# Performance work log

Hardware: AMD Instinct MI355X
Metric: run time of the kernel (lower is better)

## Reference

```python
import jax, jax.numpy as jnp
import numpy as np
from jax.scipy.special import logsumexp

D = 256; H = 8; A = D // H
B_CONST = 0.9; P_MAX = 50000.0; P_MIN = 1e-4; TANH_RATE = 0.005; EPS = 1e-10
SCALE = 1.0 / np.sqrt(D)


def setup_inputs() -> dict:
    key = jax.random.key(0)
    ks = jax.random.split(key, 5)
    B, S = 2, 512
    context = jax.random.normal(ks[0], (B, S, D), dtype=jnp.float32)
    W_Q = jax.random.normal(ks[1], (D, D), dtype=jnp.float32) * (1.0 / np.sqrt(D))
    W_KV = jax.random.normal(ks[2], (2 * D, D), dtype=jnp.float32) * (1.0 / np.sqrt(D))
    W_out = jax.random.normal(ks[3], (D, D), dtype=jnp.float32) * (1.0 / np.sqrt(D))
    p_param = jax.random.normal(ks[4], (D,), dtype=jnp.float32) * 0.02
    return {"context": context, "W_Q": W_Q, "W_KV": W_KV, "W_out": W_out, "p_param": p_param}


def reference(context, W_Q, W_KV, W_out, p_param):
    B, S, _ = context.shape
    # projections (nn.Linear: x @ W.T)
    q = context @ W_Q.T                          # [B,S,D]
    kv = context @ W_KV.T                        # [B,S,2D]
    k, v = kv[..., :D], kv[..., D:]
    # scaled p: p_max*tanh(tanh_rate*p)+1, then replace exact zeros with p_min
    p = P_MAX * jnp.tanh(TANH_RATE * p_param) + 1.0
    p = p + (p == 0).astype(p.dtype) * P_MIN
    # minmax-normalize v over the key/sequence axis into [b, 1]
    v_max = jnp.max(v, axis=-2, keepdims=True)   # [B,1,D]
    v_min = jnp.min(v, axis=-2, keepdims=True)
    v = (1.0 - B_CONST) * (v - v_min) / (v_max - v_min + EPS) + B_CONST
    z = p * jnp.log(v)                           # [B,S,D]
    # split heads
    qh = q.reshape(B, S, H, A).transpose(0, 2, 1, 3)          # [B,H,S,A]
    kh = k.reshape(B, S, H, A).transpose(0, 2, 1, 3)          # [B,H,S,A]
    zh = z.reshape(B, S, H, A).transpose(0, 2, 1, 3)[:, :, None]  # [B,H,1,K,A]
    dot = jnp.einsum('bhqa,bhka->bhqk', qh, kh)
    w = jax.nn.log_softmax(dot * SCALE, axis=-1)              # [B,H,Q,K]
    # log-domain power mean: logsumexp over keys of log-weights + p*log(v)
    mean = logsumexp(w[..., None] + zh, axis=-2)              # [B,H,Q,A]
    mean = mean.transpose(0, 2, 1, 3).reshape(B, S, D)
    e = jnp.exp(mean / p)
    # invert v minmax normalization
    e = (e - B_CONST) * (v_max - v_min + EPS) / (1.0 - B_CONST) + v_min
    return e @ W_out.T
```

## Files before the change

### kernel.cpp

```cpp
#include <hip/hip_runtime.h>
#include <math.h>

#define DD 256
#define HH 8
#define AA 32
#define SS 512
#define BB 2
constexpr float BCONST      = 0.9f;
constexpr float ONE_MINUS_B = 0.1f;
constexpr float EPSF        = 1e-10f;
constexpr float SCALEF      = 0.0625f;
constexpr float FLTMAX      = 3.402823466e38f;

#define OFF_QKV    0
#define OFF_VP     786432
#define OFF_EW     1048576
#define OFF_PMIN   1310720
#define OFF_PMAX   1318912
#define OFF_VMIN   1327104
#define OFF_VRANGE 1327616
#define OFF_P      1328128

template<int TM, int TN, int RM, int RN, bool MM>
__global__ __launch_bounds__(256) void gemm_t(
    const float* __restrict__ A, const float* __restrict__ B0,
    const float* __restrict__ B1, int nsplit,
    float* __restrict__ C, int ldc, int K, int lda,
    float* __restrict__ pminP, float* __restrict__ pmaxP) {
  constexpr int LDT = 36;
  constexpr int CG  = TN / RN;
  constexpr int NA  = TM * 32 / 1024;
  constexpr int NB  = TN * 32 / 1024;
  __shared__ float As[TM][LDT];
  __shared__ float Bs[TN][LDT];
  const int i0 = blockIdx.x * TM;
  const int j0 = blockIdx.y * TN;
  const float* Bsrc = (j0 < nsplit) ? (B0 + (size_t)j0 * K)
                                    : (B1 + (size_t)(j0 - nsplit) * K);
  const int t  = threadIdx.x;
  const int lr = t >> 3;
  const int lc = (t & 7) << 2;
  const int tx = t % CG, ty = t / CG;

  float4 pa[NA], pb[NB];
#pragma unroll
  for (int u = 0; u < NA; ++u)
    pa[u] = *(const float4*)(A + (size_t)(i0 + lr + 32 * u) * lda + lc);
#pragma unroll
  for (int u = 0; u < NB; ++u)
    pb[u] = *(const float4*)(Bsrc + (size_t)(lr + 32 * u) * K + lc);

  float acc[RM][RN] = {};
  for (int k0 = 0; k0 < K; k0 += 32) {
    __syncthreads();
#pragma unroll
    for (int u = 0; u < NA; ++u) *(float4*)&As[lr + 32 * u][lc] = pa[u];
#pragma unroll
    for (int u = 0; u < NB; ++u) *(float4*)&Bs[lr + 32 * u][lc] = pb[u];
    __syncthreads();
    if (k0 + 32 < K) {
#pragma unroll
      for (int u = 0; u < NA; ++u)
        pa[u] = *(const float4*)(A + (size_t)(i0 + lr + 32 * u) * lda + k0 + 32 + lc);
#pragma unroll
      for (int u = 0; u < NB; ++u)
        pb[u] = *(const float4*)(Bsrc + (size_t)(lr + 32 * u) * K + k0 + 32 + lc);
    }
#pragma unroll
    for (int kk = 0; kk < 32; kk += 4) {
      float4 af[RM], bf[RN];
#pragma unroll
      for (int r = 0; r < RM; ++r) af[r] = *(const float4*)&As[ty * RM + r][kk];
#pragma unroll
      for (int c = 0; c < RN; ++c) bf[c] = *(const float4*)&Bs[tx + CG * c][kk];
#pragma unroll
      for (int r = 0; r < RM; ++r)
#pragma unroll
        for (int c = 0; c < RN; ++c)
          acc[r][c] += af[r].x * bf[c].x + af[r].y * bf[c].y +
                       af[r].z * bf[c].z + af[r].w * bf[c].w;
    }
  }
#pragma unroll
  for (int r = 0; r < RM; ++r)
#pragma unroll
    for (int c = 0; c < RN; ++c)
      C[(size_t)(i0 + ty * RM + r) * ldc + j0 + tx + CG * c] = acc[r][c];

  if (MM && j0 >= 512) {
    __syncthreads();
    float* mnb = &As[0][0];
    float* mxb = &Bs[0][0];
#pragma unroll
    for (int c = 0; c < RN; ++c) {
      float mn = acc[0][c], mx = acc[0][c];
#pragma unroll
      for (int r = 1; r < RM; ++r) {
        mn = fminf(mn, acc[r][c]);
        mx = fmaxf(mx, acc[r][c]);
      }
      mnb[(tx + CG * c) * 17 + ty] = mn;
      mxb[(tx + CG * c) * 17 + ty] = mx;
    }
    __syncthreads();
    if (t < TN) {
      float mn = mnb[t * 17], mx = mxb[t * 17];
#pragma unroll
      for (int i = 1; i < 16; ++i) {
        mn = fminf(mn, mnb[t * 17 + i]);
        mx = fmaxf(mx, mxb[t * 17 + i]);
      }
      const int bx = i0 >> 5;
      pminP[bx * 256 + (j0 - 512) + t] = mn;
      pmaxP[bx * 256 + (j0 - 512) + t] = mx;
    }
  }
}

__global__ __launch_bounds__(256) void vpk(
    const float* __restrict__ qkv, const float* __restrict__ pminP,
    const float* __restrict__ pmaxP, const float* __restrict__ p_param,
    float* __restrict__ vp, float* __restrict__ vminw,
    float* __restrict__ vrangew, float* __restrict__ pw) {
  const int blk = blockIdx.x;
  const int b = blk >> 9, s = blk & 511;
  const int d = threadIdx.x;
  float mn = pminP[(b * 16) * 256 + d];
  float mx = pmaxP[(b * 16) * 256 + d];
#pragma unroll
  for (int c = 1; c < 16; ++c) {
    mn = fminf(mn, pminP[(b * 16 + c) * 256 + d]);
    mx = fmaxf(mx, pmaxP[(b * 16 + c) * 256 + d]);
  }
  float p = 50000.0f * tanhf(0.005f * p_param[d]) + 1.0f;
  if (p == 0.0f) p = 0.0001f;
  const float range = mx - mn + EPSF;
  const float v  = qkv[((size_t)(b * 512 + s)) * 768 + 512 + d];
  const float vn = (ONE_MINUS_B * (v - mn)) / range + BCONST;
  const float z  = p * logf(vn);
  vp[(size_t)blk * 256 + d] = expm1f(z);
  if (s == 0) { vminw[b * 256 + d] = mn; vrangew[b * 256 + d] = range; }
  if (blk == 0) pw[d] = p;
}

__global__ __launch_bounds__(256) void attn_k(
    const float* __restrict__ qkv, const float* __restrict__ vp,
    const float* __restrict__ pw, const float* __restrict__ vminw,
    const float* __restrict__ vrangew, float* __restrict__ ew) {
  __shared__ float qs[16][36];
  __shared__ float sc[16][516];
  __shared__ float kb[256][36];
  __shared__ float red[16][17];
  const int bh  = blockIdx.x;
  const int b   = bh >> 3, h = bh & 7;
  const int q0g = blockIdx.y * 16;
  const int t   = threadIdx.x;
  const int ldr = t >> 3, ldc4 = (t & 7) << 2;

  if (t < 128) {
    const int q = t >> 3, c4 = (t & 7) << 2;
    float4 qv = *(const float4*)(qkv + ((size_t)(b * 512 + q0g + q)) * 768 + h * 32 + c4);
    qv.x *= SCALEF; qv.y *= SCALEF; qv.z *= SCALEF; qv.w *= SCALEF;
    *(float4*)&qs[q][c4] = qv;
  }

  float4 pk[8];
#pragma unroll
  for (int u = 0; u < 8; ++u)
    pk[u] = *(const float4*)(qkv + ((size_t)(b * 512 + ldr + 32 * u)) * 768 + 256 + h * 32 + ldc4);

  const int qg = t & 3;
  const int kg = t >> 2;
  for (int kc = 0; kc < 2; ++kc) {
    __syncthreads();
#pragma unroll
    for (int u = 0; u < 8; ++u) *(float4*)&kb[ldr + 32 * u][ldc4] = pk[u];
    __syncthreads();
    if (kc == 0) {
#pragma unroll
      for (int u = 0; u < 8; ++u)
        pk[u] = *(const float4*)(qkv + ((size_t)(b * 512 + 256 + ldr + 32 * u)) * 768 + 256 + h * 32 + ldc4);
    } else {
#pragma unroll
      for (int u = 0; u < 8; ++u)
        pk[u] = *(const float4*)(vp + ((size_t)(b * 512 + ldr + 32 * u)) * 256 + h * 32 + ldc4);
    }
    float a2[4][4] = {};
#pragma unroll
    for (int kk = 0; kk < 32; kk += 4) {
      float4 qf[4], kf[4];
#pragma unroll
      for (int r = 0; r < 4; ++r) qf[r] = *(const float4*)&qs[qg * 4 + r][kk];
#pragma unroll
      for (int c = 0; c < 4; ++c) kf[c] = *(const float4*)&kb[kg + 64 * c][kk];
#pragma unroll
      for (int r = 0; r < 4; ++r)
#pragma unroll
        for (int c = 0; c < 4; ++c)
          a2[r][c] += qf[r].x * kf[c].x + qf[r].y * kf[c].y +
                      qf[r].z * kf[c].z + qf[r].w * kf[c].w;
    }
#pragma unroll
    for (int r = 0; r < 4; ++r)
#pragma unroll
      for (int c = 0; c < 4; ++c)
        sc[qg * 4 + r][kc * 256 + kg + 64 * c] = a2[r][c];
  }
  __syncthreads();

  {
    const int q = t & 15, j = t >> 4;
    float m = -FLTMAX;
#pragma unroll
    for (int i = 0; i < 32; ++i) m = fmaxf(m, sc[q][j + 16 * i]);
    red[q][j] = m;
    __syncthreads();
    float rm = red[q][0];
#pragma unroll
    for (int jj = 1; jj < 16; ++jj) rm = fmaxf(rm, red[q][jj]);
    __syncthreads();
    float ls = 0.f;
#pragma unroll
    for (int i = 0; i < 32; ++i) {
      float e = __expf(sc[q][j + 16 * i] - rm);
      sc[q][j + 16 * i] = e;
      ls += e;
    }
    red[q][j] = ls;
    __syncthreads();
    if (j == 0) {
      float tot = 0.f;
#pragma unroll
      for (int jj = 0; jj < 16; ++jj) tot += red[q][jj];
      red[q][16] = tot;
    }
  }

  float a3[4][4] = {};
  const int qg3 = t & 3;
  const int ag3 = (t >> 2) & 7;
  const int ks  = t >> 5;
  for (int kc = 0; kc < 2; ++kc) {
    __syncthreads();
#pragma unroll
    for (int u = 0; u < 8; ++u) *(float4*)&kb[ldr + 32 * u][ldc4] = pk[u];
    __syncthreads();
    if (kc == 0) {
#pragma unroll
      for (int u = 0; u < 8; ++u)
        pk[u] = *(const float4*)(vp + ((size_t)(b * 512 + 256 + ldr + 32 * u)) * 256 + h * 32 + ldc4);
    }
#pragma unroll
    for (int kk = 0; kk < 32; ++kk) {
      const int kl = ks * 32 + kk;
      const int kglob = kc * 256 + kl;
      const float4 vf = *(const float4*)&kb[kl][ag3 * 4];
      const float s0 = sc[qg3 * 4 + 0][kglob];
      const float s1 = sc[qg3 * 4 + 1][kglob];
      const float s2 = sc[qg3 * 4 + 2][kglob];
      const float s3 = sc[qg3 * 4 + 3][kglob];
      a3[0][0] += s0 * vf.x; a3[0][1] += s0 * vf.y; a3[0][2] += s0 * vf.z; a3[0][3] += s0 * vf.w;
      a3[1][0] += s1 * vf.x; a3[1][1] += s1 * vf.y; a3[1][2] += s1 * vf.z; a3[1][3] += s1 * vf.w;
      a3[2][0] += s2 * vf.x; a3[2][1] += s2 * vf.y; a3[2][2] += s2 * vf.z; a3[2][3] += s2 * vf.w;
      a3[3][0] += s3 * vf.x; a3[3][1] += s3 * vf.y; a3[3][2] += s3 * vf.z; a3[3][3] += s3 * vf.w;
    }
  }

  __syncthreads();
  float* part = &kb[0][0];
#pragma unroll
  for (int r = 0; r < 4; ++r)
#pragma unroll
    for (int c = 0; c < 4; ++c)
      part[(((qg3 * 4 + r) * 32) + ag3 * 4 + c) * 8 + ks] = a3[r][c];
  __syncthreads();
  {
    const int idx = t * 2;
    const int q = idx >> 5, a = idx & 31;
    const float invT = 1.0f / red[q][16];
    float o2[2];
#pragma unroll
    for (int o = 0; o < 2; ++o) {
      const float* p8 = part + ((size_t)(q * 32 + a + o)) * 8;
      float s = 0.f;
#pragma unroll
      for (int i = 0; i < 8; ++i) s += p8[i];
      s *= invT;
      const int d = h * 32 + a + o;
      const float p = pw[d];
      const float mean = log1pf(s);
      const float en = expf(mean / p);
      o2[o] = (en - BCONST) * vrangew[b * 256 + d] / ONE_MINUS_B + vminw[b * 256 + d];
    }
    *(float2*)(ew + ((size_t)(b * 512 + q0g + q)) * 256 + h * 32 + a) =
        make_float2(o2[0], o2[1]);
  }
}

extern "C" void kernel_launch(void* const* d_in, const int* in_sizes, int n_in,
                              void* d_out, int out_size, void* d_ws, size_t ws_size,
                              hipStream_t stream) {
  const float* ctx  = (const float*)d_in[0];
  const float* WQ   = (const float*)d_in[1];
  const float* WKV  = (const float*)d_in[2];
  const float* WOUT = (const float*)d_in[3];
  const float* PP   = (const float*)d_in[4];
  float* ws      = (float*)d_ws;
  float* qkv     = ws + OFF_QKV;
  float* vp      = ws + OFF_VP;
  float* ew      = ws + OFF_EW;
  float* pminP   = ws + OFF_PMIN;
  float* pmaxP   = ws + OFF_PMAX;
  float* vminw   = ws + OFF_VMIN;
  float* vrangew = ws + OFF_VRANGE;
  float* pw      = ws + OFF_P;
  float* out     = (float*)d_out;

  gemm_t<32, 64, 2, 4, true><<<dim3(32, 12), 256, 0, stream>>>(
      ctx, WQ, WKV, 256, qkv, 768, 256, 256, pminP, pmaxP);
  vpk<<<1024, 256, 0, stream>>>(qkv, pminP, pmaxP, PP, vp, vminw, vrangew, pw);
  attn_k<<<dim3(16, 32), 256, 0, stream>>>(qkv, vp, pw, vminw, vrangew, ew);
  gemm_t<32, 32, 2, 2, false><<<dim3(32, 8), 256, 0, stream>>>(
      ew, WOUT, WOUT, 1 << 30, out, 256, 256, 256, nullptr, nullptr);
}
```

Baseline: 123.4 us.

## Fuse v normalization into attention kernel and vectorize shared-memory score access

After: 122.9 us. About the same (-0.4%).

```diff
diff --git a/kernel.cpp b/kernel.cpp
--- a/kernel.cpp
+++ b/kernel.cpp
@@ -13,13 +13,9 @@
 constexpr float FLTMAX      = 3.402823466e38f;
 
 #define OFF_QKV    0
-#define OFF_VP     786432
-#define OFF_EW     1048576
-#define OFF_PMIN   1310720
-#define OFF_PMAX   1318912
-#define OFF_VMIN   1327104
-#define OFF_VRANGE 1327616
-#define OFF_P      1328128
+#define OFF_EW     786432
+#define OFF_PMIN   1048576
+#define OFF_PMAX   1056768
 
 template<int TM, int TN, int RM, int RN, bool MM>
 __global__ __launch_bounds__(256) void gemm_t(
@@ -117,40 +113,15 @@
   }
 }
 
-__global__ __launch_bounds__(256) void vpk(
+__global__ __launch_bounds__(256) void attn_k(
     const float* __restrict__ qkv, const float* __restrict__ pminP,
     const float* __restrict__ pmaxP, const float* __restrict__ p_param,
-    float* __restrict__ vp, float* __restrict__ vminw,
-    float* __restrict__ vrangew, float* __restrict__ pw) {
-  const int blk = blockIdx.x;
-  const int b = blk >> 9, s = blk & 511;
-  const int d = threadIdx.x;
-  float mn = pminP[(b * 16) * 256 + d];
-  float mx = pmaxP[(b * 16) * 256 + d];
-#pragma unroll
-  for (int c = 1; c < 16; ++c) {
-    mn = fminf(mn, pminP[(b * 16 + c) * 256 + d]);
-    mx = fmaxf(mx, pmaxP[(b * 16 + c) * 256 + d]);
-  }
-  float p = 50000.0f * tanhf(0.005f * p_param[d]) + 1.0f;
-  if (p == 0.0f) p = 0.0001f;
-  const float range = mx - mn + EPSF;
-  const float v  = qkv[((size_t)(b * 512 + s)) * 768 + 512 + d];
-  const float vn = (ONE_MINUS_B * (v - mn)) / range + BCONST;
-  const float z  = p * logf(vn);
-  vp[(size_t)blk * 256 + d] = expm1f(z);
-  if (s == 0) { vminw[b * 256 + d] = mn; vrangew[b * 256 + d] = range; }
-  if (blk == 0) pw[d] = p;
-}
-
-__global__ __launch_bounds__(256) void attn_k(
-    const float* __restrict__ qkv, const float* __restrict__ vp,
-    const float* __restrict__ pw, const float* __restrict__ vminw,
-    const float* __restrict__ vrangew, float* __restrict__ ew) {
+    float* __restrict__ ew) {
   __shared__ float qs[16][36];
-  __shared__ float sc[16][516];
+  __shared__ float sc[16][520];
   __shared__ float kb[256][36];
   __shared__ float red[16][17];
+  __shared__ float pl_mn[32], pl_rg[32], pl_p[32];
   const int bh  = blockIdx.x;
   const int b   = bh >> 3, h = bh & 7;
   const int q0g = blockIdx.y * 16;
@@ -163,6 +134,21 @@
     qv.x *= SCALEF; qv.y *= SCALEF; qv.z *= SCALEF; qv.w *= SCALEF;
     *(float4*)&qs[q][c4] = qv;
   }
+  if (t < 32) {
+    const int d = h * 32 + t;
+    float mn = pminP[(b * 16) * 256 + d];
+    float mx = pmaxP[(b * 16) * 256 + d];
+#pragma unroll
+    for (int c = 1; c < 16; ++c) {
+      mn = fminf(mn, pminP[(b * 16 + c) * 256 + d]);
+      mx = fmaxf(mx, pmaxP[(b * 16 + c) * 256 + d]);
+    }
+    float p = 50000.0f * tanhf(0.005f * p_param[d]) + 1.0f;
+    if (p == 0.0f) p = 0.0001f;
+    pl_mn[t] = mn;
+    pl_rg[t] = mx - mn + EPSF;
+    pl_p[t]  = p;
+  }
 
   float4 pk[8];
 #pragma unroll
@@ -183,7 +169,7 @@
     } else {
 #pragma unroll
       for (int u = 0; u < 8; ++u)
-        pk[u] = *(const float4*)(vp + ((size_t)(b * 512 + ldr + 32 * u)) * 256 + h * 32 + ldc4);
+        pk[u] = *(const float4*)(qkv + ((size_t)(b * 512 + ldr + 32 * u)) * 768 + 512 + h * 32 + ldc4);
     }
     float a2[4][4] = {};
 #pragma unroll
@@ -192,7 +178,7 @@
 #pragma unroll
       for (int r = 0; r < 4; ++r) qf[r] = *(const float4*)&qs[qg * 4 + r][kk];
 #pragma unroll
-      for (int c = 0; c < 4; ++c) kf[c] = *(const float4*)&kb[kg + 64 * c][kk];
+      for (int c = 0; c < 4; ++c) kf[c] = *(const float4*)&kb[kg * 4 + c][kk];
 #pragma unroll
       for (int r = 0; r < 4; ++r)
 #pragma unroll
@@ -202,9 +188,8 @@
     }
 #pragma unroll
     for (int r = 0; r < 4; ++r)
-#pragma unroll
-      for (int c = 0; c < 4; ++c)
-        sc[qg * 4 + r][kc * 256 + kg + 64 * c] = a2[r][c];
+      *(float4*)&sc[qg * 4 + r][kc * 256 + kg * 4] =
+          make_float4(a2[r][0], a2[r][1], a2[r][2], a2[r][3]);
   }
   __syncthreads();
 
@@ -212,7 +197,10 @@
     const int q = t & 15, j = t >> 4;
     float m = -FLTMAX;
 #pragma unroll
-    for (int i = 0; i < 32; ++i) m = fmaxf(m, sc[q][j + 16 * i]);
+    for (int g = 0; g < 8; ++g) {
+      float4 x = *(const float4*)&sc[q][j * 32 + 4 * g];
+      m = fmaxf(m, fmaxf(fmaxf(x.x, x.y), fmaxf(x.z, x.w)));
+    }
     red[q][j] = m;
     __syncthreads();
     float rm = red[q][0];
@@ -221,10 +209,12 @@
     __syncthreads();
     float ls = 0.f;
 #pragma unroll
-    for (int i = 0; i < 32; ++i) {
-      float e = __expf(sc[q][j + 16 * i] - rm);
-      sc[q][j + 16 * i] = e;
-      ls += e;
+    for (int g = 0; g < 8; ++g) {
+      float4 x = *(const float4*)&sc[q][j * 32 + 4 * g];
+      x.x = __expf(x.x - rm); x.y = __expf(x.y - rm);
+      x.z = __expf(x.z - rm); x.w = __expf(x.w - rm);
+      *(float4*)&sc[q][j * 32 + 4 * g] = x;
+      ls += x.x + x.y + x.z + x.w;
     }
     red[q][j] = ls;
     __syncthreads();
@@ -243,26 +233,41 @@
   for (int kc = 0; kc < 2; ++kc) {
     __syncthreads();
 #pragma unroll
-    for (int u = 0; u < 8; ++u) *(float4*)&kb[ldr + 32 * u][ldc4] = pk[u];
+    for (int u = 0; u < 8; ++u) {
+      const float4 vv = pk[u];
+      float4 tv;
+      tv.x = expm1f(pl_p[ldc4 + 0] * logf((ONE_MINUS_B * (vv.x - pl_mn[ldc4 + 0])) / pl_rg[ldc4 + 0] + BCONST));
+      tv.y = expm1f(pl_p[ldc4 + 1] * logf((ONE_MINUS_B * (vv.y - pl_mn[ldc4 + 1])) / pl_rg[ldc4 + 1] + BCONST));
+      tv.z = expm1f(pl_p[ldc4 + 2] * logf((ONE_MINUS_B * (vv.z - pl_mn[ldc4 + 2])) / pl_rg[ldc4 + 2] + BCONST));
+      tv.w = expm1f(pl_p[ldc4 + 3] * logf((ONE_MINUS_B * (vv.w - pl_mn[ldc4 + 3])) / pl_rg[ldc4 + 3] + BCONST));
+      *(float4*)&kb[ldr + 32 * u][ldc4] = tv;
+    }
     __syncthreads();
     if (kc == 0) {
 #pragma unroll
       for (int u = 0; u < 8; ++u)
-        pk[u] = *(const float4*)(vp + ((size_t)(b * 512 + 256 + ldr + 32 * u)) * 256 + h * 32 + ldc4);
-    }
-#pragma unroll
-    for (int kk = 0; kk < 32; ++kk) {
-      const int kl = ks * 32 + kk;
-      const int kglob = kc * 256 + kl;
-      const float4 vf = *(const float4*)&kb[kl][ag3 * 4];
-      const float s0 = sc[qg3 * 4 + 0][kglob];
-      const float s1 = sc[qg3 * 4 + 1][kglob];
-      const float s2 = sc[qg3 * 4 + 2][kglob];
-      const float s3 = sc[qg3 * 4 + 3][kglob];
-      a3[0][0] += s0 * vf.x; a3[0][1] += s0 * vf.y; a3[0][2] += s0 * vf.z; a3[0][3] += s0 * vf.w;
-      a3[1][0] += s1 * vf.x; a3[1][1] += s1 * vf.y; a3[1][2] += s1 * vf.z; a3[1][3] += s1 * vf.w;
-      a3[2][0] += s2 * vf.x; a3[2][1] += s2 * vf.y; a3[2][2] += s2 * vf.z; a3[2][3] += s2 * vf.w;
-      a3[3][0] += s3 * vf.x; a3[3][1] += s3 * vf.y; a3[3][2] += s3 * vf.z; a3[3][3] += s3 * vf.w;
+        pk[u] = *(const float4*)(qkv + ((size_t)(b * 512 + 256 + ldr + 32 * u)) * 768 + 512 + h * 32 + ldc4);
+    }
+#pragma unroll
+    for (int g = 0; g < 8; ++g) {
+      const int k0 = ks * 32 + g * 4;
+      float4 s4[4], vf[4];
+#pragma unroll
+      for (int r = 0; r < 4; ++r)
+        s4[r] = *(const float4*)&sc[qg3 * 4 + r][kc * 256 + k0];
+#pragma unroll
+      for (int c = 0; c < 4; ++c)
+        vf[c] = *(const float4*)&kb[k0 + c][ag3 * 4];
+#pragma unroll
+      for (int r = 0; r < 4; ++r) {
+        const float* sp = (const float*)&s4[r];
+#pragma unroll
+        for (int c = 0; c < 4; ++c) {
+          const float sv = sp[c];
+          a3[r][0] += sv * vf[c].x; a3[r][1] += sv * vf[c].y;
+          a3[r][2] += sv * vf[c].z; a3[r][3] += sv * vf[c].w;
+        }
+      }
     }
   }
 
@@ -286,11 +291,10 @@
 #pragma unroll
       for (int i = 0; i < 8; ++i) s += p8[i];
       s *= invT;
-      const int d = h * 32 + a + o;
-      const float p = pw[d];
+      const float p = pl_p[a + o];
       const float mean = log1pf(s);
       const float en = expf(mean / p);
-      o2[o] = (en - BCONST) * vrangew[b * 256 + d] / ONE_MINUS_B + vminw[b * 256 + d];
+      o2[o] = (en - BCONST) * pl_rg[a + o] / ONE_MINUS_B + pl_mn[a + o];
     }
     *(float2*)(ew + ((size_t)(b * 512 + q0g + q)) * 256 + h * 32 + a) =
         make_float2(o2[0], o2[1]);
@@ -305,21 +309,16 @@
   const float* WKV  = (const float*)d_in[2];
   const float* WOUT = (const float*)d_in[3];
   const float* PP   = (const float*)d_in[4];
-  float* ws      = (float*)d_ws;
-  float* qkv     = ws + OFF_QKV;
-  float* vp      = ws + OFF_VP;
-  float* ew      = ws + OFF_EW;
-  float* pminP   = ws + OFF_PMIN;
-  float* pmaxP   = ws + OFF_PMAX;
-  float* vminw   = ws + OFF_VMIN;
-  float* vrangew = ws + OFF_VRANGE;
-  float* pw      = ws + OFF_P;
-  float* out     = (float*)d_out;
+  float* ws    = (float*)d_ws;
+  float* qkv   = ws + OFF_QKV;
+  float* ew    = ws + OFF_EW;
+  float* pminP = ws + OFF_PMIN;
+  float* pmaxP = ws + OFF_PMAX;
+  float* out   = (float*)d_out;
 
   gemm_t<32, 64, 2, 4, true><<<dim3(32, 12), 256, 0, stream>>>(
       ctx, WQ, WKV, 256, qkv, 768, 256, 256, pminP, pmaxP);
-  vpk<<<1024, 256, 0, stream>>>(qkv, pminP, pmaxP, PP, vp, vminw, vrangew, pw);
-  attn_k<<<dim3(16, 32), 256, 0, stream>>>(qkv, vp, pw, vminw, vrangew, ew);
+  attn_k<<<dim3(16, 32), 256, 0, stream>>>(qkv, pminP, pmaxP, PP, ew);
   gemm_t<32, 32, 2, 2, false><<<dim3(32, 8), 256, 0, stream>>>(
       ew, WOUT, WOUT, 1 << 30, out, 256, 256, 256, nullptr, nullptr);
 }
```

## Swizzle K/V shared tile, transpose score buffer, shuffle-reduce partial sums

Applied to the files above, without the earlier changes.

Result: no change. 124.6 us (+1.0%).

```diff
diff --git a/kernel.cpp b/kernel.cpp
--- a/kernel.cpp
+++ b/kernel.cpp
@@ -20,6 +20,9 @@
 #define OFF_VMIN   1327104
 #define OFF_VRANGE 1327616
 #define OFF_P      1328128
+
+#define KB4(buf, row, col4) \
+  (&(buf)[((row) << 5) | ((((col4) >> 2) ^ (((row) >> 2) & 7)) << 2)])
 
 template<int TM, int TN, int RM, int RN, bool MM>
 __global__ __launch_bounds__(256) void gemm_t(
@@ -137,8 +140,7 @@
   const float range = mx - mn + EPSF;
   const float v  = qkv[((size_t)(b * 512 + s)) * 768 + 512 + d];
   const float vn = (ONE_MINUS_B * (v - mn)) / range + BCONST;
-  const float z  = p * logf(vn);
-  vp[(size_t)blk * 256 + d] = expm1f(z);
+  vp[(size_t)blk * 256 + d] = expm1f(p * logf(vn));
   if (s == 0) { vminw[b * 256 + d] = mn; vrangew[b * 256 + d] = range; }
   if (blk == 0) pw[d] = p;
 }
@@ -148,8 +150,8 @@
     const float* __restrict__ pw, const float* __restrict__ vminw,
     const float* __restrict__ vrangew, float* __restrict__ ew) {
   __shared__ float qs[16][36];
-  __shared__ float sc[16][516];
-  __shared__ float kb[256][36];
+  __shared__ float scT[512 * 20];
+  __shared__ float kb[256 * 32];
   __shared__ float red[16][17];
   const int bh  = blockIdx.x;
   const int b   = bh >> 3, h = bh & 7;
@@ -174,7 +176,7 @@
   for (int kc = 0; kc < 2; ++kc) {
     __syncthreads();
 #pragma unroll
-    for (int u = 0; u < 8; ++u) *(float4*)&kb[ldr + 32 * u][ldc4] = pk[u];
+    for (int u = 0; u < 8; ++u) *(float4*)KB4(kb, ldr + 32 * u, ldc4) = pk[u];
     __syncthreads();
     if (kc == 0) {
 #pragma unroll
@@ -192,7 +194,7 @@
 #pragma unroll
       for (int r = 0; r < 4; ++r) qf[r] = *(const float4*)&qs[qg * 4 + r][kk];
 #pragma unroll
-      for (int c = 0; c < 4; ++c) kf[c] = *(const float4*)&kb[kg + 64 * c][kk];
+      for (int c = 0; c < 4; ++c) kf[c] = *(const float4*)KB4(kb, kg * 4 + c, kk);
 #pragma unroll
       for (int r = 0; r < 4; ++r)
 #pragma unroll
@@ -201,10 +203,9 @@
                       qf[r].z * kf[c].z + qf[r].w * kf[c].w;
     }
 #pragma unroll
-    for (int r = 0; r < 4; ++r)
-#pragma unroll
-      for (int c = 0; c < 4; ++c)
-        sc[qg * 4 + r][kc * 256 + kg + 64 * c] = a2[r][c];
+    for (int c = 0; c < 4; ++c)
+      *(float4*)&scT[(kc * 256 + kg * 4 + c) * 20 + qg * 4] =
+          make_float4(a2[0][c], a2[1][c], a2[2][c], a2[3][c]);
   }
   __syncthreads();
 
@@ -212,7 +213,7 @@
     const int q = t & 15, j = t >> 4;
     float m = -FLTMAX;
 #pragma unroll
-    for (int i = 0; i < 32; ++i) m = fmaxf(m, sc[q][j + 16 * i]);
+    for (int i = 0; i < 32; ++i) m = fmaxf(m, scT[(j * 32 + i) * 20 + q]);
     red[q][j] = m;
     __syncthreads();
     float rm = red[q][0];
@@ -222,8 +223,8 @@
     float ls = 0.f;
 #pragma unroll
     for (int i = 0; i < 32; ++i) {
-      float e = __expf(sc[q][j + 16 * i] - rm);
-      sc[q][j + 16 * i] = e;
+      float e = __expf(scT[(j * 32 + i) * 20 + q] - rm);
+      scT[(j * 32 + i) * 20 + q] = e;
       ls += e;
     }
     red[q][j] = ls;
@@ -243,7 +244,7 @@
   for (int kc = 0; kc < 2; ++kc) {
     __syncthreads();
 #pragma unroll
-    for (int u = 0; u < 8; ++u) *(float4*)&kb[ldr + 32 * u][ldc4] = pk[u];
+    for (int u = 0; u < 8; ++u) *(float4*)KB4(kb, ldr + 32 * u, ldc4) = pk[u];
     __syncthreads();
     if (kc == 0) {
 #pragma unroll
@@ -251,40 +252,44 @@
         pk[u] = *(const float4*)(vp + ((size_t)(b * 512 + 256 + ldr + 32 * u)) * 256 + h * 32 + ldc4);
     }
 #pragma unroll
-    for (int kk = 0; kk < 32; ++kk) {
-      const int kl = ks * 32 + kk;
-      const int kglob = kc * 256 + kl;
-      const float4 vf = *(const float4*)&kb[kl][ag3 * 4];
-      const float s0 = sc[qg3 * 4 + 0][kglob];
-      const float s1 = sc[qg3 * 4 + 1][kglob];
-      const float s2 = sc[qg3 * 4 + 2][kglob];
-      const float s3 = sc[qg3 * 4 + 3][kglob];
-      a3[0][0] += s0 * vf.x; a3[0][1] += s0 * vf.y; a3[0][2] += s0 * vf.z; a3[0][3] += s0 * vf.w;
-      a3[1][0] += s1 * vf.x; a3[1][1] += s1 * vf.y; a3[1][2] += s1 * vf.z; a3[1][3] += s1 * vf.w;
-      a3[2][0] += s2 * vf.x; a3[2][1] += s2 * vf.y; a3[2][2] += s2 * vf.z; a3[2][3] += s2 * vf.w;
-      a3[3][0] += s3 * vf.x; a3[3][1] += s3 * vf.y; a3[3][2] += s3 * vf.z; a3[3][3] += s3 * vf.w;
-    }
-  }
-
+    for (int g = 0; g < 8; ++g) {
+#pragma unroll
+      for (int c = 0; c < 4; ++c) {
+        const int k = ks * 32 + g * 4 + c;
+        const float4 sq = *(const float4*)&scT[(kc * 256 + k) * 20 + qg3 * 4];
+        const float4 vf = *(const float4*)KB4(kb, k, ag3 * 4);
+        a3[0][0] += sq.x * vf.x; a3[0][1] += sq.x * vf.y; a3[0][2] += sq.x * vf.z; a3[0][3] += sq.x * vf.w;
+        a3[1][0] += sq.y * vf.x; a3[1][1] += sq.y * vf.y; a3[1][2] += sq.y * vf.z; a3[1][3] += sq.y * vf.w;
+        a3[2][0] += sq.z * vf.x; a3[2][1] += sq.z * vf.y; a3[2][2] += sq.z * vf.z; a3[2][3] += sq.z * vf.w;
+        a3[3][0] += sq.w * vf.x; a3[3][1] += sq.w * vf.y; a3[3][2] += sq.w * vf.z; a3[3][3] += sq.w * vf.w;
+      }
+    }
+  }
+
+#pragma unroll
+  for (int r = 0; r < 4; ++r)
+#pragma unroll
+    for (int c = 0; c < 4; ++c)
+      a3[r][c] += __shfl_xor(a3[r][c], 32);
   __syncthreads();
-  float* part = &kb[0][0];
-#pragma unroll
-  for (int r = 0; r < 4; ++r)
-#pragma unroll
-    for (int c = 0; c < 4; ++c)
-      part[(((qg3 * 4 + r) * 32) + ag3 * 4 + c) * 8 + ks] = a3[r][c];
+  float* part2 = &kb[0];
+  if ((t & 32) == 0) {
+    const int w = t >> 6;
+#pragma unroll
+    for (int r = 0; r < 4; ++r)
+#pragma unroll
+      for (int c = 0; c < 4; ++c)
+        part2[w * 520 + (qg3 * 4 + r) * 32 + ag3 * 4 + c] = a3[r][c];
+  }
   __syncthreads();
   {
-    const int idx = t * 2;
-    const int q = idx >> 5, a = idx & 31;
+    const int q = t >> 4, a = (t * 2) & 31;
     const float invT = 1.0f / red[q][16];
     float o2[2];
 #pragma unroll
     for (int o = 0; o < 2; ++o) {
-      const float* p8 = part + ((size_t)(q * 32 + a + o)) * 8;
-      float s = 0.f;
-#pragma unroll
-      for (int i = 0; i < 8; ++i) s += p8[i];
+      const int ia = q * 32 + a + o;
+      float s = part2[ia] + part2[520 + ia] + part2[1040 + ia] + part2[1560 + ia];
       s *= invT;
       const int d = h * 32 + a + o;
       const float p = pw[d];
```
